# Optimization experiments

Hardware: AMD Instinct MI355X
Metric: run time of the kernel (lower is better)

## Reference

```python
import jax, jax.numpy as jnp
import numpy as np
from jax import lax

IN_CH = 512
OUT_CH = 512
HEAD_DIM = 8
NUM_HEADS = IN_CH // HEAD_DIM  # 64
INNER = NUM_HEADS * HEAD_DIM   # 512
KSIZE = 5
EPS = 1e-15
BN_EPS = 1e-5
DN = ('NCHW', 'OIHW', 'NCHW')


def setup_inputs() -> dict:
    key = jax.random.key(0)
    ks = jax.random.split(key, 10)
    s = 0.02
    return {
        'hidden_states': jax.random.normal(ks[0], (4, IN_CH, 64, 64), jnp.float32),
        'wq': jax.random.normal(ks[1], (INNER, IN_CH), jnp.float32) * s,
        'wk': jax.random.normal(ks[2], (INNER, IN_CH), jnp.float32) * s,
        'wv': jax.random.normal(ks[3], (INNER, IN_CH), jnp.float32) * s,
        # depthwise conv: groups = 3*INNER, 1 in-channel per group
        'dw_kernel': jax.random.normal(ks[4], (3 * INNER, 1, KSIZE, KSIZE), jnp.float32) * s,
        # grouped 1x1 conv: groups = 3*NUM_HEADS -> 3*INNER/(3*NUM_HEADS)=HEAD_DIM in-ch/group
        'pw_kernel': jax.random.normal(ks[5], (3 * INNER, HEAD_DIM, 1, 1), jnp.float32) * s,
        # proj_out 1x1: in = INNER*(1+len(kernel_sizes)) = 2*INNER
        'proj_kernel': jax.random.normal(ks[6], (OUT_CH, 2 * INNER, 1, 1), jnp.float32) * s,
        'bn_gamma': jnp.ones((OUT_CH,), jnp.float32),
        'bn_beta': jnp.zeros((OUT_CH,), jnp.float32),
        'bn_mean': jnp.zeros((OUT_CH,), jnp.float32),
        'bn_var': jnp.ones((OUT_CH,), jnp.float32),
    }


def _forward(hidden_states, wq, wk, wv, dw_kernel, pw_kernel, proj_kernel,
             bn_gamma, bn_beta, bn_mean, bn_var):
    x = hidden_states  # [B,C,H,W]
    B, _, H, W = x.shape
    h = jnp.moveaxis(x, 1, -1)  # [B,H,W,C]
    q = h @ wq.T
    k = h @ wk.T
    v = h @ wv.T
    qkv = jnp.moveaxis(jnp.concatenate([q, k, v], axis=-1), -1, 1)  # [B,3*INNER,H,W]

    # multi-scale aggregation: depthwise 5x5 then grouped 1x1
    dw = lax.conv_general_dilated(qkv, dw_kernel, (1, 1), 'SAME',
                                  feature_group_count=3 * INNER, dimension_numbers=DN)
    pw = lax.conv_general_dilated(dw, pw_kernel, (1, 1), 'VALID',
                                  feature_group_count=3 * NUM_HEADS, dimension_numbers=DN)
    qkv_all = jnp.concatenate([qkv, pw], axis=1)  # [B, 2*3*INNER, H, W]

    # relu linear attention (fp32)
    N = H * W
    d = HEAD_DIM
    f = qkv_all.astype(jnp.float32).reshape(B, -1, 3 * d, N)  # [B, nh_total, 3d, N]
    query = jax.nn.relu(f[:, :, :d])
    key_ = jax.nn.relu(f[:, :, d:2 * d])
    value = f[:, :, 2 * d:]
    value_pad = jnp.concatenate([value, jnp.ones_like(value[:, :, :1])], axis=2)  # [B,nh,d+1,N]
    scores = jnp.einsum('bhdn,bhen->bhde', value_pad, key_)   # [B,nh,d+1,d]
    out = jnp.einsum('bhde,bhen->bhdn', scores, query)         # [B,nh,d+1,N]
    out = out[:, :, :-1] / (out[:, :, -1:] + EPS)
    out = out.reshape(B, -1, H, W).astype(qkv_all.dtype)        # [B, 2*INNER, H, W]

    # proj_out 1x1 conv + BatchNorm2d (eval mode, running stats)
    y = lax.conv_general_dilated(out, proj_kernel, (1, 1), 'VALID', dimension_numbers=DN)
    inv = bn_gamma / jnp.sqrt(bn_var + BN_EPS)
    y = y * inv[None, :, None, None] + (bn_beta - bn_mean * inv)[None, :, None, None]
    return y + x


def reference(hidden_states, wq, wk, wv, dw_kernel, pw_kernel, proj_kernel,
              bn_gamma, bn_beta, bn_mean, bn_var):
    return _forward(hidden_states, wq, wk, wv, dw_kernel, pw_kernel, proj_kernel,
                    bn_gamma, bn_beta, bn_mean, bn_var)
```

## Files before the change

kernel.cpp:

```cpp
#include <hip/hip_runtime.h>
#include <hip/hip_bf16.h>

typedef __hip_bfloat16 bf16;
typedef __attribute__((ext_vector_type(8))) short bf16x8;
typedef __attribute__((ext_vector_type(4))) float f32x4;

#define BATCH 4
#define CIN   512
#define HW    64
#define NPIX  4096
#define CALL  3072
#define NHEAD 128
#define EPS_LITE 1e-15f
#define BN_EPS   1e-5f


__device__ __forceinline__ short f2bf(float f) {
    __hip_bfloat16 h = __float2bfloat16(f);
    short s; __builtin_memcpy(&s, &h, 2); return s;
}
__device__ __forceinline__ float bfl(unsigned u) {
    unsigned v = u << 16; float f; __builtin_memcpy(&f, &v, 4); return f;
}
__device__ __forceinline__ float bfh(unsigned u) {
    unsigned v = u & 0xffff0000u; float f; __builtin_memcpy(&f, &v, 4); return f;
}
__device__ __forceinline__ unsigned packbf(float a, float b) {
    return (unsigned)(unsigned short)f2bf(a) | ((unsigned)(unsigned short)f2bf(b) << 16);
}
__device__ __forceinline__ void gll16(const void* gsrc, void* ldst) {
    __builtin_amdgcn_global_load_lds(
        (const __attribute__((address_space(1))) unsigned int*)gsrc,
        (__attribute__((address_space(3))) unsigned int*)ldst, 16, 0, 0);
}

__global__ __launch_bounds__(256) void k_cvtw(const float* __restrict__ wq,
                                              const float* __restrict__ wk,
                                              const float* __restrict__ wv,
                                              const float* __restrict__ pj,
                                              bf16* __restrict__ Wbf,
                                              bf16* __restrict__ Pbf) {
    const int e = (blockIdx.x * 256 + threadIdx.x) * 4;
    const float* s; bf16* dst;
    if (e < 786432) {
        int o;
        if (e < 262144)      { s = wq; o = e; }
        else if (e < 524288) { s = wk; o = e - 262144; }
        else                 { s = wv; o = e - 524288; }
        f32x4 v = *(const f32x4*)(s + o);
        dst = Wbf + e;
        *(ushort2*)dst = make_ushort2((unsigned short)f2bf(v[0]), (unsigned short)f2bf(v[1]));
        *(ushort2*)(dst + 2) = make_ushort2((unsigned short)f2bf(v[2]), (unsigned short)f2bf(v[3]));
    } else {
        const int o = e - 786432;
        f32x4 v = *(const f32x4*)(pj + o);
        dst = Pbf + o;
        *(ushort2*)dst = make_ushort2((unsigned short)f2bf(v[0]), (unsigned short)f2bf(v[1]));
        *(ushort2*)(dst + 2) = make_ushort2((unsigned short)f2bf(v[2]), (unsigned short)f2bf(v[3]));
    }
}

__global__ __launch_bounds__(256) void k_cvtx(const float* __restrict__ x,
                                              bf16* __restrict__ xT) {
    __shared__ short lds[64][72];
    const int t   = threadIdx.x;
    const int px0 = blockIdx.x * 64;
    const int k0  = blockIdx.y * 64;
    const int b   = blockIdx.z;

    const int pr = t & 15, rr = t >> 4;
#pragma unroll
    for (int it = 0; it < 4; ++it) {
        const int row = it * 16 + rr;
        f32x4 v = *(const f32x4*)(x + (size_t)(b * CIN + k0 + row) * NPIX + px0 + pr * 4);
#pragma unroll
        for (int i = 0; i < 4; ++i) lds[pr * 4 + i][row] = f2bf(v[i]);
    }
    __syncthreads();

    const int px = t >> 2, kc = t & 3;
    uint4 u0 = *(const uint4*)&lds[px][kc * 16];
    uint4 u1 = *(const uint4*)&lds[px][kc * 16 + 8];
    bf16* dst = xT + ((size_t)b * NPIX + px0 + px) * 512 + k0 + kc * 16;
    *(uint4*)dst = u0;
    *(uint4*)(dst + 8) = u1;
}

template<int KD, int MT, bool PROJ>
__global__ __launch_bounds__(256) void k_gemm3(
        const bf16* __restrict__ Xt,
        const bf16* __restrict__ Wb,
        bf16* __restrict__ Obf,
        const float* __restrict__ gm, const float* __restrict__ bt,
        const float* __restrict__ mu, const float* __restrict__ va,
        const float* __restrict__ resid, float* __restrict__ Of)
{
    constexpr int NT = KD / 32;
    constexpr int MS = MT / 32;
    constexpr int AG = MT / 64;
    __shared__ short Ald[2][MT * 32];
    __shared__ short Bld[2][128 * 32];

    const int t    = threadIdx.x;
    const int lane = t & 63;
    const int w    = t >> 6;
    const int wm   = w >> 1, wn = w & 1;
    const int n0   = blockIdx.x * 128;
    const int c0   = blockIdx.y * MT;
    const int b    = blockIdx.z;

    const bf16* abase = Wb + (size_t)(c0 + w * (MT / 4) + (lane >> 2)) * KD + (lane & 3) * 8;
    const bf16* bbase = Xt + ((size_t)b * NPIX + n0 + w * 32 + (lane >> 2)) * KD + (lane & 3) * 8;

    auto stage = [&](int s, int buf) {
#pragma unroll
        for (int q = 0; q < AG; ++q)
            gll16(abase + (size_t)q * 16 * KD + s * 32,
                  &Ald[buf][(w * (MT / 4) + q * 16) * 32]);
#pragma unroll
        for (int q = 0; q < 2; ++q)
            gll16(bbase + (size_t)q * 16 * KD + s * 32,
                  &Bld[buf][(w * 32 + q * 16) * 32]);
    };

    f32x4 acc[MS][4];
#pragma unroll
    for (int ms = 0; ms < MS; ++ms)
#pragma unroll
        for (int ns = 0; ns < 4; ++ns)
#pragma unroll
            for (int j = 0; j < 4; ++j) acc[ms][ns][j] = 0.f;

    stage(0, 0);
    __syncthreads();

    const int l15 = lane & 15, l4 = lane >> 4;
    for (int s = 0; s < NT; ++s) {
        const int cur = s & 1;
        if (s + 1 < NT) stage(s + 1, cur ^ 1);

        bf16x8 af[MS], bv[4];
#pragma unroll
        for (int ms = 0; ms < MS; ++ms)
            af[ms] = *(const bf16x8*)&Ald[cur][(wm * (MT / 2) + ms * 16 + l15) * 32 + l4 * 8];
#pragma unroll
        for (int ns = 0; ns < 4; ++ns)
            bv[ns] = *(const bf16x8*)&Bld[cur][(wn * 64 + ns * 16 + l15) * 32 + l4 * 8];
#pragma unroll
        for (int ms = 0; ms < MS; ++ms)
#pragma unroll
            for (int ns = 0; ns < 4; ++ns)
                acc[ms][ns] = __builtin_amdgcn_mfma_f32_16x16x32_bf16(
                    af[ms], bv[ns], acc[ms][ns], 0, 0, 0);

        __syncthreads();
    }

    if (!PROJ) {
#pragma unroll
        for (int ms = 0; ms < MS; ++ms) {
            const int crow = c0 + wm * (MT / 2) + ms * 16 + l4 * 4;
#pragma unroll
            for (int ns = 0; ns < 4; ++ns) {
                const int ncol = n0 + wn * 64 + ns * 16 + l15;
#pragma unroll
                for (int j = 0; j < 4; ++j) {
                    bf16 h; short sv = f2bf(acc[ms][ns][j]);
                    __builtin_memcpy(&h, &sv, 2);
                    Obf[((size_t)b * CALL + crow + j) * NPIX + ncol] = h;
                }
            }
        }
    } else {
#pragma unroll
        for (int ms = 0; ms < MS; ++ms) {
            const int crow = c0 + wm * (MT / 2) + ms * 16 + l4 * 4;
#pragma unroll
            for (int j = 0; j < 4; ++j) {
                const int o = crow + j;
                const float inv = gm[o] / sqrtf(va[o] + BN_EPS);
                const float sh  = bt[o] - mu[o] * inv;
#pragma unroll
                for (int ns = 0; ns < 4; ++ns) {
                    const int ncol = n0 + wn * 64 + ns * 16 + l15;
                    const size_t idx = ((size_t)b * 512 + o) * NPIX + ncol;
                    Of[idx] = acc[ms][ns][j] * inv + sh + resid[idx];
                }
            }
        }
    }
}

#define DW_ICS (36 * 80)
#define DW_DCS (32 * 64)
__global__ __launch_bounds__(512) void k_dwpw(const float* __restrict__ dwk,
                                              const float* __restrict__ pwk,
                                              bf16* __restrict__ qkv_all) {
    __shared__ short in_lds[8 * DW_ICS];
    __shared__ short dw_lds[8 * DW_DCS];

    const int t  = threadIdx.x;
    const int g  = blockIdx.y;
    const int b  = blockIdx.z;
    const int y0 = blockIdx.x * 32;

    const bf16* src = qkv_all + ((size_t)b * CALL + g * 8) * NPIX;
#pragma unroll
    for (int i = 0; i < 6; ++i) {
        const int v = i * 512 + t;
        if (v < 2880) {
            const int ch  = v / 360;
            const int rem = v % 360;
            const int row = rem / 10;
            const int seg = rem % 10;
            const int grow = y0 + row - 2;
            uint4 val = make_uint4(0u, 0u, 0u, 0u);
            if (seg >= 1 && seg <= 8 && grow >= 0 && grow < HW)
                val = *(const uint4*)(src + (size_t)ch * NPIX + grow * HW + (seg - 1) * 8);
            *(uint4*)&in_lds[ch * DW_ICS + row * 80 + seg * 8] = val;
        }
    }

    const int lane = t & 63;
    const int w    = t >> 6;
    const int xb   = lane & 7;
    const int ch   = lane >> 3;
    const int x0   = xb * 8;

    float kc[25];
    {
        const float* kp = dwk + (size_t)(g * 8 + ch) * 25;
#pragma unroll
        for (int i = 0; i < 25; ++i) kc[i] = kp[i];
    }
    __syncthreads();

    float A[5][12];
    const short* cb = &in_lds[ch * DW_ICS + x0];

    auto loadrow = [&](int L, float* f) {
        const short* rp = cb + L * 80;
        uint2 lo = *(const uint2*)(rp + 4);
        uint4 md = *(const uint4*)(rp + 8);
        uint2 hi = *(const uint2*)(rp + 16);
        f[0]  = bfl(lo.y); f[1]  = bfh(lo.y);
        f[2]  = bfl(md.x); f[3]  = bfh(md.x);
        f[4]  = bfl(md.y); f[5]  = bfh(md.y);
        f[6]  = bfl(md.z); f[7]  = bfh(md.z);
        f[8]  = bfl(md.w); f[9]  = bfh(md.w);
        f[10] = bfl(hi.x); f[11] = bfh(hi.x);
    };

    const int r0 = w * 4;
    loadrow(r0 + 0, A[0]);
    loadrow(r0 + 1, A[1]);
    loadrow(r0 + 2, A[2]);
    loadrow(r0 + 3, A[3]);

#pragma unroll
    for (int ri = 0; ri < 4; ++ri) {
        loadrow(r0 + ri + 4, A[(ri + 4) % 5]);
        float acc[8];
#pragma unroll
        for (int i = 0; i < 8; ++i) acc[i] = 0.f;
#pragma unroll
        for (int dy = 0; dy < 5; ++dy) {
            const float* Ar = A[(ri + dy) % 5];
#pragma unroll
            for (int dx = 0; dx < 5; ++dx) {
                const float kv = kc[dy * 5 + dx];
#pragma unroll
                for (int i = 0; i < 8; ++i)
                    acc[i] += Ar[i + dx] * kv;
            }
        }
        uint4 pk;
        pk.x = packbf(acc[0], acc[1]);
        pk.y = packbf(acc[2], acc[3]);
        pk.z = packbf(acc[4], acc[5]);
        pk.w = packbf(acc[6], acc[7]);
        *(uint4*)&dw_lds[ch * DW_DCS + (r0 + ri) * 64 + x0] = pk;
    }
    __syncthreads();

    const float* pwb = pwk + (size_t)g * 64;
#pragma unroll
    for (int it = 0; it < 2; ++it) {
        const int p2 = (it * 512 + t) * 2;
        float v0[8], v1[8];
#pragma unroll
        for (int ci = 0; ci < 8; ++ci) {
            const unsigned u = *(const unsigned*)&dw_lds[ci * DW_DCS + p2];
            v0[ci] = bfl(u); v1[ci] = bfh(u);
        }
        bf16* op = qkv_all + ((size_t)b * CALL + 1536 + g * 8) * NPIX + y0 * HW + p2;
#pragma unroll
        for (int o = 0; o < 8; ++o) {
            float s0 = 0.f, s1 = 0.f;
#pragma unroll
            for (int ci = 0; ci < 8; ++ci) {
                const float wv = pwb[o * 8 + ci];
                s0 += wv * v0[ci]; s1 += wv * v1[ci];
            }
            *(unsigned*)(op + (size_t)o * NPIX) = packbf(s0, s1);
        }
    }
}

__global__ __launch_bounds__(64) void k_scores(const bf16* __restrict__ qkv_all,
                                               float* __restrict__ part) {
    const int lane = threadIdx.x;
    const int h = blockIdx.y;
    const int b = blockIdx.z;
    const bf16* base = qkv_all + ((size_t)b * CALL + h * 24) * NPIX;

    float acc[72];
#pragma unroll
    for (int i = 0; i < 72; ++i) acc[i] = 0.f;

    for (int it = 0; it < 4; ++it) {
        const int n = blockIdx.x * 512 + it * 128 + lane * 2;
        const bf16* p = base + n;
        float k0[8], k1[8], v0[8], v1[8];
#pragma unroll
        for (int e = 0; e < 8; ++e) {
            const unsigned u = *(const unsigned*)&p[(size_t)(8 + e) * NPIX];
            k0[e] = fmaxf(bfl(u), 0.f); k1[e] = fmaxf(bfh(u), 0.f);
        }
#pragma unroll
        for (int d = 0; d < 8; ++d) {
            const unsigned u = *(const unsigned*)&p[(size_t)(16 + d) * NPIX];
            v0[d] = bfl(u); v1[d] = bfh(u);
        }
#pragma unroll
        for (int d = 0; d < 9; ++d) {
            const float vd0 = (d < 8) ? v0[d] : 1.f;
            const float vd1 = (d < 8) ? v1[d] : 1.f;
#pragma unroll
            for (int e = 0; e < 8; ++e)
                acc[d * 8 + e] += vd0 * k0[e] + vd1 * k1[e];
        }
    }

    const int bh = b * NHEAD + h;
#pragma unroll
    for (int i = 0; i < 72; ++i) {
        float v = acc[i];
        for (int off = 32; off; off >>= 1) v += __shfl_xor(v, off, 64);
        if (lane == 0) part[((size_t)bh * 72 + i) * 8 + blockIdx.x] = v;
    }
}

__global__ __launch_bounds__(256) void k_att3(const bf16* __restrict__ qkv_all,
                                              const float* __restrict__ part,
                                              bf16* __restrict__ attT) {
    __shared__ float sc[72];
    const int t  = threadIdx.x;
    const int h  = blockIdx.y;
    const int b  = blockIdx.z;
    const int bh = b * NHEAD + h;

    if (t < 72) {
        float s = 0.f;
#pragma unroll
        for (int ns = 0; ns < 8; ++ns) s += part[((size_t)bh * 72 + t) * 8 + ns];
        sc[t] = s;
    }
    __syncthreads();

    const int px = blockIdx.x * 256 + t;
    const bf16* qb = qkv_all + ((size_t)b * CALL + h * 24) * NPIX + px;
    float q[8];
#pragma unroll
    for (int e = 0; e < 8; ++e)
        q[e] = fmaxf(__bfloat162float(qb[(size_t)e * NPIX]), 0.f);

    float num[9];
#pragma unroll
    for (int d = 0; d < 9; ++d) {
        float s = 0.f;
#pragma unroll
        for (int e = 0; e < 8; ++e) s += sc[d * 8 + e] * q[e];
        num[d] = s;
    }
    const float inv = 1.f / (num[8] + EPS_LITE);
    uint4 pk;
    pk.x = packbf(num[0] * inv, num[1] * inv);
    pk.y = packbf(num[2] * inv, num[3] * inv);
    pk.z = packbf(num[4] * inv, num[5] * inv);
    pk.w = packbf(num[6] * inv, num[7] * inv);
    *(uint4*)(attT + ((size_t)b * NPIX + px) * 1024 + h * 8) = pk;
}

extern "C" void kernel_launch(void* const* d_in, const int* in_sizes, int n_in,
                              void* d_out, int out_size, void* d_ws, size_t ws_size,
                              hipStream_t stream) {
    const float* x   = (const float*)d_in[0];
    const float* wq  = (const float*)d_in[1];
    const float* wk  = (const float*)d_in[2];
    const float* wv  = (const float*)d_in[3];
    const float* dwk = (const float*)d_in[4];
    const float* pwk = (const float*)d_in[5];
    const float* pj  = (const float*)d_in[6];
    const float* gm  = (const float*)d_in[7];
    const float* bt  = (const float*)d_in[8];
    const float* mu  = (const float*)d_in[9];
    const float* va  = (const float*)d_in[10];
    float* out = (float*)d_out;

    char* ws = (char*)d_ws;
    bf16*  qkv_all = (bf16*)(ws);
    bf16*  attT    = (bf16*)(ws + 100663296);
    bf16*  xT      = (bf16*)(ws + 100663296);
    float* part    = (float*)(ws + 134217728);
    bf16*  Wbf     = (bf16*)(ws + 135544832);
    bf16*  Pbf     = (bf16*)(ws + 137117696);

    k_cvtw<<<dim3(1280), 256, 0, stream>>>(wq, wk, wv, pj, Wbf, Pbf);
    k_cvtx<<<dim3(64, 8, BATCH), 256, 0, stream>>>(x, xT);
    k_gemm3<512, 128, false><<<dim3(32, 12, BATCH), 256, 0, stream>>>(
        xT, Wbf, qkv_all, nullptr, nullptr, nullptr, nullptr, nullptr, nullptr);
    k_dwpw  <<<dim3( 2, 192, BATCH), 512, 0, stream>>>(dwk, pwk, qkv_all);
    k_scores<<<dim3( 8, 128, BATCH),  64, 0, stream>>>(qkv_all, part);
    k_att3  <<<dim3(16, 128, BATCH), 256, 0, stream>>>(qkv_all, part, attT);
    k_gemm3<1024, 64, true><<<dim3(32, 8, BATCH), 256, 0, stream>>>(
        attT, Pbf, nullptr, gm, bt, mu, va, x, out);
}
```

Before: 182.6 us.

## Fuse conversion kernels, swizzle GEMM block order, read dwconv input from global

Merges the weight and activation bf16 conversion kernels into one launch, saving a kernel launch. Both GEMMs now use a 1D grid with an XCD-aware swizzle so that neighbouring blocks share weight and pixel tiles, aiming at better L2 locality. The depthwise conv drops its LDS halo staging and loads each row directly from global memory with boundary masking, using smaller 256-thread blocks over 16 rows, and the pointwise conv uses packed float2 math. Workspace pointers are shifted by 4 KB; direct global loads may re-read overlapping halo rows.

```diff
diff --git a/kernel.cpp b/kernel.cpp
--- a/kernel.cpp
+++ b/kernel.cpp
@@ -4,6 +4,7 @@
 typedef __hip_bfloat16 bf16;
 typedef __attribute__((ext_vector_type(8))) short bf16x8;
 typedef __attribute__((ext_vector_type(4))) float f32x4;
+typedef __attribute__((ext_vector_type(2))) float f32v2;
 
 #define BATCH 4
 #define CIN   512
@@ -34,59 +35,62 @@
         (__attribute__((address_space(3))) unsigned int*)ldst, 16, 0, 0);
 }
 
-__global__ __launch_bounds__(256) void k_cvtw(const float* __restrict__ wq,
-                                              const float* __restrict__ wk,
-                                              const float* __restrict__ wv,
-                                              const float* __restrict__ pj,
-                                              bf16* __restrict__ Wbf,
-                                              bf16* __restrict__ Pbf) {
-    const int e = (blockIdx.x * 256 + threadIdx.x) * 4;
-    const float* s; bf16* dst;
-    if (e < 786432) {
-        int o;
-        if (e < 262144)      { s = wq; o = e; }
-        else if (e < 524288) { s = wk; o = e - 262144; }
-        else                 { s = wv; o = e - 524288; }
-        f32x4 v = *(const f32x4*)(s + o);
-        dst = Wbf + e;
-        *(ushort2*)dst = make_ushort2((unsigned short)f2bf(v[0]), (unsigned short)f2bf(v[1]));
-        *(ushort2*)(dst + 2) = make_ushort2((unsigned short)f2bf(v[2]), (unsigned short)f2bf(v[3]));
+__global__ __launch_bounds__(256) void k_cvt(const float* __restrict__ x,
+                                             const float* __restrict__ wq,
+                                             const float* __restrict__ wk,
+                                             const float* __restrict__ wv,
+                                             const float* __restrict__ pj,
+                                             bf16* __restrict__ xT,
+                                             bf16* __restrict__ Wbf,
+                                             bf16* __restrict__ Pbf) {
+    __shared__ short lds[64][72];
+    const int bid = blockIdx.x;
+    const int t   = threadIdx.x;
+
+    if (bid < 2048) {
+        const int px0 = (bid & 63) * 64;
+        const int k0  = ((bid >> 6) & 7) * 64;
+        const int b   = bid >> 9;
+
+        const int pr = t & 15, rr = t >> 4;
+#pragma unroll
+        for (int it = 0; it < 4; ++it) {
+            const int row = it * 16 + rr;
+            f32x4 v = *(const f32x4*)(x + (size_t)(b * CIN + k0 + row) * NPIX + px0 + pr * 4);
+#pragma unroll
+            for (int i = 0; i < 4; ++i) lds[pr * 4 + i][row] = f2bf(v[i]);
+        }
+        __syncthreads();
+
+        const int px = t >> 2, kc = t & 3;
+        uint4 u0 = *(const uint4*)&lds[px][kc * 16];
+        uint4 u1 = *(const uint4*)&lds[px][kc * 16 + 8];
+        bf16* dst = xT + ((size_t)b * NPIX + px0 + px) * 512 + k0 + kc * 16;
+        *(uint4*)dst = u0;
+        *(uint4*)(dst + 8) = u1;
     } else {
-        const int o = e - 786432;
-        f32x4 v = *(const f32x4*)(pj + o);
-        dst = Pbf + o;
-        *(ushort2*)dst = make_ushort2((unsigned short)f2bf(v[0]), (unsigned short)f2bf(v[1]));
-        *(ushort2*)(dst + 2) = make_ushort2((unsigned short)f2bf(v[2]), (unsigned short)f2bf(v[3]));
-    }
-}
-
-__global__ __launch_bounds__(256) void k_cvtx(const float* __restrict__ x,
-                                              bf16* __restrict__ xT) {
-    __shared__ short lds[64][72];
-    const int t   = threadIdx.x;
-    const int px0 = blockIdx.x * 64;
-    const int k0  = blockIdx.y * 64;
-    const int b   = blockIdx.z;
-
-    const int pr = t & 15, rr = t >> 4;
-#pragma unroll
-    for (int it = 0; it < 4; ++it) {
-        const int row = it * 16 + rr;
-        f32x4 v = *(const f32x4*)(x + (size_t)(b * CIN + k0 + row) * NPIX + px0 + pr * 4);
-#pragma unroll
-        for (int i = 0; i < 4; ++i) lds[pr * 4 + i][row] = f2bf(v[i]);
-    }
-    __syncthreads();
-
-    const int px = t >> 2, kc = t & 3;
-    uint4 u0 = *(const uint4*)&lds[px][kc * 16];
-    uint4 u1 = *(const uint4*)&lds[px][kc * 16 + 8];
-    bf16* dst = xT + ((size_t)b * NPIX + px0 + px) * 512 + k0 + kc * 16;
-    *(uint4*)dst = u0;
-    *(uint4*)(dst + 8) = u1;
-}
-
-template<int KD, int MT, bool PROJ>
+        const int e = ((bid - 2048) * 256 + t) * 4;
+        const float* s; bf16* dst;
+        if (e < 786432) {
+            int o;
+            if (e < 262144)      { s = wq; o = e; }
+            else if (e < 524288) { s = wk; o = e - 262144; }
+            else                 { s = wv; o = e - 524288; }
+            f32x4 v = *(const f32x4*)(s + o);
+            dst = Wbf + e;
+            *(ushort2*)dst = make_ushort2((unsigned short)f2bf(v[0]), (unsigned short)f2bf(v[1]));
+            *(ushort2*)(dst + 2) = make_ushort2((unsigned short)f2bf(v[2]), (unsigned short)f2bf(v[3]));
+        } else {
+            const int o = e - 786432;
+            f32x4 v = *(const f32x4*)(pj + o);
+            dst = Pbf + o;
+            *(ushort2*)dst = make_ushort2((unsigned short)f2bf(v[0]), (unsigned short)f2bf(v[1]));
+            *(ushort2*)(dst + 2) = make_ushort2((unsigned short)f2bf(v[2]), (unsigned short)f2bf(v[3]));
+        }
+    }
+}
+
+template<int KD, int MT, int NC, bool PROJ>
 __global__ __launch_bounds__(256) void k_gemm3(
         const bf16* __restrict__ Xt,
         const bf16* __restrict__ Wb,
@@ -98,16 +102,22 @@
     constexpr int NT = KD / 32;
     constexpr int MS = MT / 32;
     constexpr int AG = MT / 64;
+    constexpr int NWG = NC * 32 * BATCH;
     __shared__ short Ald[2][MT * 32];
     __shared__ short Bld[2][128 * 32];
+
+    const int id = blockIdx.x;
+    const int sw = (id & 7) * (NWG / 8) + (id >> 3);
+    const int ct = sw % NC;
+    const int nb = sw / NC;
+    const int n0 = (nb & 31) << 7;
+    const int b  = nb >> 5;
+    const int c0 = ct * MT;
 
     const int t    = threadIdx.x;
     const int lane = t & 63;
     const int w    = t >> 6;
     const int wm   = w >> 1, wn = w & 1;
-    const int n0   = blockIdx.x * 128;
-    const int c0   = blockIdx.y * MT;
-    const int b    = blockIdx.z;
 
     const bf16* abase = Wb + (size_t)(c0 + w * (MT / 4) + (lane >> 2)) * KD + (lane & 3) * 8;
     const bf16* bbase = Xt + ((size_t)b * NPIX + n0 + w * 32 + (lane >> 2)) * KD + (lane & 3) * 8;
@@ -191,35 +201,16 @@
     }
 }
 
-#define DW_ICS (36 * 80)
-#define DW_DCS (32 * 64)
-__global__ __launch_bounds__(512) void k_dwpw(const float* __restrict__ dwk,
+#define DW_DCS 1032
+__global__ __launch_bounds__(256) void k_dwpw(const float* __restrict__ dwk,
                                               const float* __restrict__ pwk,
                                               bf16* __restrict__ qkv_all) {
-    __shared__ short in_lds[8 * DW_ICS];
-    __shared__ short dw_lds[8 * DW_DCS];
+    __shared__ short dlds[8 * DW_DCS];
 
     const int t  = threadIdx.x;
     const int g  = blockIdx.y;
     const int b  = blockIdx.z;
-    const int y0 = blockIdx.x * 32;
-
-    const bf16* src = qkv_all + ((size_t)b * CALL + g * 8) * NPIX;
-#pragma unroll
-    for (int i = 0; i < 6; ++i) {
-        const int v = i * 512 + t;
-        if (v < 2880) {
-            const int ch  = v / 360;
-            const int rem = v % 360;
-            const int row = rem / 10;
-            const int seg = rem % 10;
-            const int grow = y0 + row - 2;
-            uint4 val = make_uint4(0u, 0u, 0u, 0u);
-            if (seg >= 1 && seg <= 8 && grow >= 0 && grow < HW)
-                val = *(const uint4*)(src + (size_t)ch * NPIX + grow * HW + (seg - 1) * 8);
-            *(uint4*)&in_lds[ch * DW_ICS + row * 80 + seg * 8] = val;
-        }
-    }
+    const int y0 = blockIdx.x * 16;
 
     const int lane = t & 63;
     const int w    = t >> 6;
@@ -227,39 +218,46 @@
     const int ch   = lane >> 3;
     const int x0   = xb * 8;
 
+    const bf16* src = qkv_all + ((size_t)b * CALL + g * 8 + ch) * NPIX;
+
     float kc[25];
     {
         const float* kp = dwk + (size_t)(g * 8 + ch) * 25;
 #pragma unroll
         for (int i = 0; i < 25; ++i) kc[i] = kp[i];
     }
-    __syncthreads();
-
+
+    const int r0 = w * 4;
     float A[5][12];
-    const short* cb = &in_lds[ch * DW_ICS + x0];
-
-    auto loadrow = [&](int L, float* f) {
-        const short* rp = cb + L * 80;
-        uint2 lo = *(const uint2*)(rp + 4);
-        uint4 md = *(const uint4*)(rp + 8);
-        uint2 hi = *(const uint2*)(rp + 16);
-        f[0]  = bfl(lo.y); f[1]  = bfh(lo.y);
+
+    auto loadrow = [&](int rel, float* f) {
+        const int gy = y0 + r0 + rel - 2;
+        unsigned lou = 0, hiu = 0;
+        uint4 md = make_uint4(0u, 0u, 0u, 0u);
+        if (gy >= 0 && gy < HW) {
+            const bf16* rp = src + gy * HW + x0;
+            lou = *(const unsigned*)(rp - 2);
+            md  = *(const uint4*)(rp);
+            hiu = *(const unsigned*)(rp + 8);
+            if (xb == 0) lou = 0;
+            if (xb == 7) hiu = 0;
+        }
+        f[0]  = bfl(lou); f[1]  = bfh(lou);
         f[2]  = bfl(md.x); f[3]  = bfh(md.x);
         f[4]  = bfl(md.y); f[5]  = bfh(md.y);
         f[6]  = bfl(md.z); f[7]  = bfh(md.z);
         f[8]  = bfl(md.w); f[9]  = bfh(md.w);
-        f[10] = bfl(hi.x); f[11] = bfh(hi.x);
+        f[10] = bfl(hiu); f[11] = bfh(hiu);
     };
 
-    const int r0 = w * 4;
-    loadrow(r0 + 0, A[0]);
-    loadrow(r0 + 1, A[1]);
-    loadrow(r0 + 2, A[2]);
-    loadrow(r0 + 3, A[3]);
+    loadrow(0, A[0]);
+    loadrow(1, A[1]);
+    loadrow(2, A[2]);
+    loadrow(3, A[3]);
 
 #pragma unroll
     for (int ri = 0; ri < 4; ++ri) {
-        loadrow(r0 + ri + 4, A[(ri + 4) % 5]);
+        loadrow(ri + 4, A[(ri + 4) % 5]);
         float acc[8];
 #pragma unroll
         for (int i = 0; i < 8; ++i) acc[i] = 0.f;
@@ -279,30 +277,28 @@
         pk.y = packbf(acc[2], acc[3]);
         pk.z = packbf(acc[4], acc[5]);
         pk.w = packbf(acc[6], acc[7]);
-        *(uint4*)&dw_lds[ch * DW_DCS + (r0 + ri) * 64 + x0] = pk;
+        *(uint4*)&dlds[ch * DW_DCS + (r0 + ri) * 64 + x0] = pk;
     }
     __syncthreads();
 
     const float* pwb = pwk + (size_t)g * 64;
 #pragma unroll
-    for (int it = 0; it < 2; ++it) {
-        const int p2 = (it * 512 + t) * 2;
-        float v0[8], v1[8];
+    for (int it2 = 0; it2 < 2; ++it2) {
+        const int p2 = (it2 * 256 + t) * 2;
+        f32v2 v2[8];
 #pragma unroll
         for (int ci = 0; ci < 8; ++ci) {
-            const unsigned u = *(const unsigned*)&dw_lds[ci * DW_DCS + p2];
-            v0[ci] = bfl(u); v1[ci] = bfh(u);
+            const unsigned u = *(const unsigned*)&dlds[ci * DW_DCS + p2];
+            v2[ci][0] = bfl(u); v2[ci][1] = bfh(u);
         }
         bf16* op = qkv_all + ((size_t)b * CALL + 1536 + g * 8) * NPIX + y0 * HW + p2;
 #pragma unroll
         for (int o = 0; o < 8; ++o) {
-            float s0 = 0.f, s1 = 0.f;
-#pragma unroll
-            for (int ci = 0; ci < 8; ++ci) {
-                const float wv = pwb[o * 8 + ci];
-                s0 += wv * v0[ci]; s1 += wv * v1[ci];
-            }
-            *(unsigned*)(op + (size_t)o * NPIX) = packbf(s0, s1);
+            f32v2 s2 = {0.f, 0.f};
+#pragma unroll
+            for (int ci = 0; ci < 8; ++ci)
+                s2 += pwb[o * 8 + ci] * v2[ci];
+            *(unsigned*)(op + (size_t)o * NPIX) = packbf(s2[0], s2[1]);
         }
     }
 }
@@ -409,20 +405,19 @@
     float* out = (float*)d_out;
 
     char* ws = (char*)d_ws;
-    bf16*  qkv_all = (bf16*)(ws);
-    bf16*  attT    = (bf16*)(ws + 100663296);
-    bf16*  xT      = (bf16*)(ws + 100663296);
-    float* part    = (float*)(ws + 134217728);
-    bf16*  Wbf     = (bf16*)(ws + 135544832);
-    bf16*  Pbf     = (bf16*)(ws + 137117696);
-
-    k_cvtw<<<dim3(1280), 256, 0, stream>>>(wq, wk, wv, pj, Wbf, Pbf);
-    k_cvtx<<<dim3(64, 8, BATCH), 256, 0, stream>>>(x, xT);
-    k_gemm3<512, 128, false><<<dim3(32, 12, BATCH), 256, 0, stream>>>(
+    bf16*  qkv_all = (bf16*)(ws + 4096);
+    bf16*  attT    = (bf16*)(ws + 100667392);
+    bf16*  xT      = (bf16*)(ws + 100667392);
+    float* part    = (float*)(ws + 134221824);
+    bf16*  Wbf     = (bf16*)(ws + 135548928);
+    bf16*  Pbf     = (bf16*)(ws + 137121792);
+
+    k_cvt<<<dim3(3328), 256, 0, stream>>>(x, wq, wk, wv, pj, xT, Wbf, Pbf);
+    k_gemm3<512, 128, 12, false><<<dim3(1536), 256, 0, stream>>>(
         xT, Wbf, qkv_all, nullptr, nullptr, nullptr, nullptr, nullptr, nullptr);
-    k_dwpw  <<<dim3( 2, 192, BATCH), 512, 0, stream>>>(dwk, pwk, qkv_all);
+    k_dwpw  <<<dim3( 4, 192, BATCH), 256, 0, stream>>>(dwk, pwk, qkv_all);
     k_scores<<<dim3( 8, 128, BATCH),  64, 0, stream>>>(qkv_all, part);
     k_att3  <<<dim3(16, 128, BATCH), 256, 0, stream>>>(qkv_all, part, attT);
-    k_gemm3<1024, 64, true><<<dim3(32, 8, BATCH), 256, 0, stream>>>(
+    k_gemm3<1024, 64, 8, true><<<dim3(1024), 256, 0, stream>>>(
         attT, Pbf, nullptr, gm, bt, mu, va, x, out);
 }
```

Result: faster. 177.5 us (-2.8%).
